# Kernel optimization log

Hardware: AMD Instinct MI355X
Metric: run time of the kernel (lower is better)

The kernel has to match this reference:

```python
import jax, jax.numpy as jnp
import numpy as np

NUM_GRAPHS = 1024  # static number of segments for global_mean_pool


def setup_inputs() -> dict:
    key = jax.random.key(0)
    ks = jax.random.split(key, 16)
    N, E, F_IN, H = 100000, 1000000, 32, 64
    NUM_ATOM, NUM_ACT, L = 16, 8, 3
    s = 0.05
    x = jax.random.normal(ks[0], (N, F_IN), dtype=jnp.float32)
    edge_index = jax.random.randint(ks[1], (2, E), 0, N, dtype=jnp.int64)
    batch = jnp.sort(jax.random.randint(ks[2], (N,), 0, NUM_GRAPHS, dtype=jnp.int64))
    W_emb = jax.random.normal(ks[3], (F_IN, H), dtype=jnp.float32) * s
    b_emb = jnp.zeros((H,), dtype=jnp.float32)
    W_convs = jax.random.normal(ks[4], (L, H, H), dtype=jnp.float32) * s
    b_convs = jnp.zeros((L, H), dtype=jnp.float32)
    W_act = jax.random.normal(ks[5], (H, NUM_ACT), dtype=jnp.float32) * s
    b_act = jnp.zeros((NUM_ACT,), dtype=jnp.float32)
    W_tgt = jax.random.normal(ks[6], (H, 1), dtype=jnp.float32) * s
    b_tgt = jnp.zeros((1,), dtype=jnp.float32)
    W_atom = jax.random.normal(ks[7], (H, NUM_ATOM), dtype=jnp.float32) * s
    b_atom = jnp.zeros((NUM_ATOM,), dtype=jnp.float32)
    return {"x": x, "edge_index": edge_index, "batch": batch,
            "W_emb": W_emb, "b_emb": b_emb, "W_convs": W_convs, "b_convs": b_convs,
            "W_act": W_act, "b_act": b_act, "W_tgt": W_tgt, "b_tgt": b_tgt,
            "W_atom": W_atom, "b_atom": b_atom}


def reference(x, edge_index, batch, W_emb, b_emb, W_convs, b_convs,
              W_act, b_act, W_tgt, b_tgt, W_atom, b_atom):
    N = x.shape[0]
    # --- GCN normalization with self-loops (PyG GCNConv default) ---
    self_idx = jnp.arange(N, dtype=edge_index.dtype)
    src = jnp.concatenate([edge_index[0], self_idx])  # message source (row)
    dst = jnp.concatenate([edge_index[1], self_idx])  # aggregation target (col)
    ones_e = jnp.ones(src.shape[0], dtype=x.dtype)
    deg = jax.ops.segment_sum(ones_e, dst, num_segments=N)  # in-degree + self-loop
    dinv = jnp.where(deg > 0, jax.lax.rsqrt(deg), 0.0)
    norm = (dinv[src] * dinv[dst])[:, None]  # [E+N, 1]

    h = jax.nn.relu(x @ W_emb + b_emb)  # node embedding
    for i in range(W_convs.shape[0]):
        m = (h @ W_convs[i])[src] * norm            # gather + scale
        agg = jax.ops.segment_sum(m, dst, num_segments=N)  # scatter-add
        h = jax.nn.relu(agg + b_convs[i])

    # --- global mean pool over graphs ---
    cnt = jax.ops.segment_sum(jnp.ones(N, dtype=x.dtype), batch, num_segments=NUM_GRAPHS)
    pooled = jax.ops.segment_sum(h, batch, num_segments=NUM_GRAPHS)
    pooled = pooled / jnp.maximum(cnt, 1.0)[:, None]

    action_type_logits = pooled @ W_act + b_act            # [G, num_action_types]
    target_node_logits = (h @ W_tgt + b_tgt)[:, 0]         # [N]
    new_atom_type_logits = pooled @ W_atom + b_atom        # [G, num_atom_types]
    return (action_type_logits, target_node_logits, new_atom_type_logits, h)
```

## Files before the change

kernel.cpp:

```cpp
#include <hip/hip_runtime.h>
#include <hip/hip_fp16.h>

#define HD 64
#define FIN 32
#define NG 1024
#define STRIDE 64
#define SLOT0 4
#define DEGCAP 59
#define SH 72

typedef _Float16 f16x8 __attribute__((ext_vector_type(8)));
typedef float f32x4 __attribute__((ext_vector_type(4)));

__device__ __forceinline__ int fmap(int jt, int c) {
    return (jt < 2) ? (2 * c + jt) : (32 + 2 * c + (jt - 2));
}

__device__ __forceinline__ void nt_store_h2(__half2 v, __half2* p) {
    __builtin_nontemporal_store(*(int*)&v, (int*)p);
}

__global__ __launch_bounds__(256) void k_prep(int* __restrict__ col,
                                              __half2* __restrict__ BaZR,
                                              __half2* __restrict__ BbZR,
                                              const float* __restrict__ Wconv,
                                              __half* __restrict__ Wf, int wtotal,
                                              const float* __restrict__ Wemb,
                                              __half* __restrict__ Wef, int N) {
    int b = blockIdx.x, t = threadIdx.x;
    int v = b * 256 + t;
    if (v < N) col[(size_t)v << 6] = 0;
    if (b < 48) {
        int tid = b * 256 + t;
        if (tid < wtotal) {
            int layer = tid >> 12;
            int r = tid & 4095;
            int frag = r >> 9, lane = (r >> 3) & 63, e = r & 7;
            int jt = frag >> 1, kh = frag & 1;
            int k = kh * 32 + (lane >> 4) * 8 + e;
            int n = fmap(jt, lane & 15);
            Wf[tid] = (_Float16)Wconv[(size_t)layer * 4096 + k * 64 + n];
        }
    } else if (b < 56) {
        int tid = (b - 48) * 256 + t;
        if (tid < 2048) {
            int jt = tid >> 9, lane = (tid >> 3) & 63, e = tid & 7;
            int k = (lane >> 4) * 8 + e;
            int n = fmap(jt, lane & 15);
            Wef[tid] = (_Float16)Wemb[k * HD + n];
        }
    } else if (b == 56) {
        __half2 z = __floats2half2_rn(0.f, 0.f);
        if (t < 32) BaZR[t] = z;
        else if (t < 64) BbZR[t - 32] = z;
    }
}

__global__ void k_fill(const int* __restrict__ src, const int* __restrict__ dst,
                       int* __restrict__ col, int E) {
    int e = blockIdx.x * blockDim.x + threadIdx.x;
    if (e < E) {
        int d = dst[e];
        int pos = atomicAdd(&col[(size_t)d << 6], 1);
        if (pos < STRIDE - SLOT0) col[((size_t)d << 6) + SLOT0 + pos] = src[e];
    }
}

__device__ __forceinline__ void gemm_from_lds(const __half* hs, const float* dvs,
                                              const float4* __restrict__ Wf4,
                                              __half2* __restrict__ Bout,
                                              int node0, int N, int t) {
    int lane = t & 63;
    int wv = t >> 6;
    int lm = lane & 15, kq = lane >> 4;
    union U { float4 f; f16x8 h; };
    U a0, a1;
    const __half* hrow = hs + (size_t)(wv * 16 + lm) * SH;
    a0.f = *(const float4*)(hrow + kq * 8);
    a1.f = *(const float4*)(hrow + 32 + kq * 8);
    f32x4 acc[4];
#pragma unroll
    for (int jt = 0; jt < 4; jt++) acc[jt] = (f32x4){0.f, 0.f, 0.f, 0.f};
#pragma unroll
    for (int jt = 0; jt < 4; jt++) {
        U b0, b1;
        b0.f = Wf4[(jt * 2 + 0) * 64 + lane];
        b1.f = Wf4[(jt * 2 + 1) * 64 + lane];
        acc[jt] = __builtin_amdgcn_mfma_f32_16x16x32_f16(a0.h, b0.h, acc[jt], 0, 0, 0);
        acc[jt] = __builtin_amdgcn_mfma_f32_16x16x32_f16(a1.h, b1.h, acc[jt], 0, 0, 0);
    }
#pragma unroll
    for (int r = 0; r < 4; r++) {
        int lv = wv * 16 + kq * 4 + r;
        int v = node0 + lv;
        if (v < N) {
            float dv = dvs[lv];
            nt_store_h2(__floats2half2_rn(acc[0][r] * dv, acc[1][r] * dv),
                        Bout + (size_t)v * 32 + lm);
            nt_store_h2(__floats2half2_rn(acc[2][r] * dv, acc[3][r] * dv),
                        Bout + (size_t)v * 32 + 16 + lm);
        }
    }
}

__global__ __launch_bounds__(256) void k_emb_gemm0(const float* __restrict__ x,
                                                   const float4* __restrict__ Wef4,
                                                   const float* __restrict__ bemb,
                                                   const int* __restrict__ col,
                                                   const float4* __restrict__ Wf0,
                                                   __half2* __restrict__ Bout, int N) {
    __shared__ __half hs[64 * SH];
    __shared__ float dvs[64];
    int t = threadIdx.x;
    int lane = t & 63;
    int wv = t >> 6;
    int node0 = blockIdx.x * 64;
    int nodew = node0 + wv * 16;
    int m = lane & 15, kq = lane >> 4;

    int vm = nodew + m;
    if (vm > N - 1) vm = N - 1;
    const float4* xr = (const float4*)(x + (size_t)vm * FIN + kq * 8);
    float4 xa = xr[0], xb = xr[1];
    f16x8 a;
    a[0] = (_Float16)xa.x; a[1] = (_Float16)xa.y; a[2] = (_Float16)xa.z; a[3] = (_Float16)xa.w;
    a[4] = (_Float16)xb.x; a[5] = (_Float16)xb.y; a[6] = (_Float16)xb.z; a[7] = (_Float16)xb.w;

    union U { float4 f; f16x8 h; };
    f32x4 acc[4];
#pragma unroll
    for (int jt = 0; jt < 4; jt++) {
        U b; b.f = Wef4[jt * 64 + lane];
        acc[jt] = (f32x4){0.f, 0.f, 0.f, 0.f};
        acc[jt] = __builtin_amdgcn_mfma_f32_16x16x32_f16(a, b.h, acc[jt], 0, 0, 0);
    }
    float b01x = bemb[2 * m], b01y = bemb[2 * m + 1];
    float b23x = bemb[32 + 2 * m], b23y = bemb[32 + 2 * m + 1];
    __half2 z = __floats2half2_rn(0.f, 0.f);
#pragma unroll
    for (int r = 0; r < 4; r++) {
        int lv = wv * 16 + kq * 4 + r;
        int v = node0 + lv;
        __half2 p01 = z, p23 = z;
        if (v < N) {
            p01 = __floats2half2_rn(fmaxf(acc[0][r] + b01x, 0.f),
                                    fmaxf(acc[1][r] + b01y, 0.f));
            p23 = __floats2half2_rn(fmaxf(acc[2][r] + b23x, 0.f),
                                    fmaxf(acc[3][r] + b23y, 0.f));
        }
        *(__half2*)(hs + (size_t)lv * SH + 2 * m) = p01;
        *(__half2*)(hs + (size_t)lv * SH + 32 + 2 * m) = p23;
        if (m == 0)
            dvs[lv] = (v < N) ? rsqrtf((float)(col[(size_t)v << 6] + 1)) : 1.f;
    }
    __syncthreads();
    gemm_from_lds(hs, dvs, Wf0, Bout, node0, N, t);
}

__global__ __launch_bounds__(256) void k_layer(const __half2* __restrict__ Bin,
                                               const int* __restrict__ col,
                                               const float* __restrict__ bias,
                                               const float4* __restrict__ Wnext,
                                               __half2* __restrict__ Bout,
                                               int N, int ZR) {
    __shared__ __half hs[64 * SH];
    __shared__ float dvs[64];
    int t = threadIdx.x;
    int lane = t & 63;
    int wv = t >> 6;
    int node0 = blockIdx.x * 64;
    int q = lane >> 4, p = lane & 15;
    float4 b4 = *(const float4*)(bias + 4 * p);

#pragma unroll
    for (int pass = 0; pass < 4; pass++) {
        int lv = wv * 16 + pass * 4 + q;
        int v = node0 + lv;
        int vc = (v < N) ? v : 0;
        const int* bucket = col + ((size_t)vc << 6);
        int degraw = bucket[0];
        int deg = degraw > DEGCAP ? DEGCAP : degraw;
        int dmax = deg;
        dmax = max(dmax, __shfl_xor(dmax, 16, 64));
        dmax = max(dmax, __shfl_xor(dmax, 32, 64));
        int rounds = (dmax + 4) >> 2;

        float2 a0 = make_float2(0.f, 0.f), a1 = make_float2(0.f, 0.f);
        for (int rd = 0; rd < rounds; rd++) {
            int4 iq = *(const int4*)(bucket + SLOT0 + rd * 4);
            int idx[4] = {iq.x, iq.y, iq.z, iq.w};
#pragma unroll
            for (int r = 0; r < 4; r++) {
                int i = rd * 4 + r;
                idx[r] = (i < deg) ? idx[r] : ((i == deg) ? vc : ZR);
            }
            float2 raw[4];
#pragma unroll
            for (int r = 0; r < 4; r++)
                raw[r] = *(const float2*)(Bin + (size_t)idx[r] * 32 + p * 2);
#pragma unroll
            for (int r = 0; r < 4; r++) {
                float2 f0 = __half22float2(((const __half2*)&raw[r])[0]);
                float2 f1 = __half22float2(((const __half2*)&raw[r])[1]);
                a0.x += f0.x; a0.y += f0.y; a1.x += f1.x; a1.y += f1.y;
            }
        }
        float dv = rsqrtf((float)(degraw + 1));
        float r0 = fmaxf(dv * a0.x + b4.x, 0.f);
        float r1 = fmaxf(dv * a0.y + b4.y, 0.f);
        float r2 = fmaxf(dv * a1.x + b4.z, 0.f);
        float r3 = fmaxf(dv * a1.y + b4.w, 0.f);
        if (v >= N) { r0 = r1 = r2 = r3 = 0.f; dv = 1.f; }
        __half* hrow = hs + (size_t)lv * SH + 4 * p;
        *(__half2*)(hrow) = __floats2half2_rn(r0, r1);
        *(__half2*)(hrow + 2) = __floats2half2_rn(r2, r3);
        if (p == 0) dvs[lv] = dv;
    }
    __syncthreads();
    gemm_from_lds(hs, dvs, Wnext, Bout, node0, N, t);
}

__global__ __launch_bounds__(256) void k_gather_last(const __half2* __restrict__ Bin,
                                                     const int* __restrict__ col,
                                                     const float* __restrict__ bias,
                                                     float* __restrict__ hout,
                                                     const float* __restrict__ Wtgt,
                                                     const float* __restrict__ btgt,
                                                     float* __restrict__ tgt,
                                                     int N, int ZR) {
    int t = threadIdx.x;
    int lane = t & 63;
    int wv = t >> 6;
    int q = lane >> 4, p = lane & 15;
    int v = blockIdx.x * 16 + wv * 4 + q;
    if (v >= N) return;

    const int* bucket = col + ((size_t)v << 6);
    int degraw = bucket[0];
    int deg = degraw > DEGCAP ? DEGCAP : degraw;
    int dmax = deg;
    dmax = max(dmax, __shfl_xor(dmax, 16, 64));
    dmax = max(dmax, __shfl_xor(dmax, 32, 64));
    int rounds = (dmax + 4) >> 2;

    float2 a0 = make_float2(0.f, 0.f), a1 = make_float2(0.f, 0.f);
    for (int rd = 0; rd < rounds; rd++) {
        int4 iq = *(const int4*)(bucket + SLOT0 + rd * 4);
        int idx[4] = {iq.x, iq.y, iq.z, iq.w};
#pragma unroll
        for (int r = 0; r < 4; r++) {
            int i = rd * 4 + r;
            idx[r] = (i < deg) ? idx[r] : ((i == deg) ? v : ZR);
        }
        float2 raw[4];
#pragma unroll
        for (int r = 0; r < 4; r++)
            raw[r] = *(const float2*)(Bin + (size_t)idx[r] * 32 + p * 2);
#pragma unroll
        for (int r = 0; r < 4; r++) {
            float2 f0 = __half22float2(((const __half2*)&raw[r])[0]);
            float2 f1 = __half22float2(((const __half2*)&raw[r])[1]);
            a0.x += f0.x; a0.y += f0.y; a1.x += f1.x; a1.y += f1.y;
        }
    }
    float dv = rsqrtf((float)(degraw + 1));
    float4 b4 = *(const float4*)(bias + 4 * p);
    float r0 = fmaxf(dv * a0.x + b4.x, 0.f);
    float r1 = fmaxf(dv * a0.y + b4.y, 0.f);
    float r2 = fmaxf(dv * a1.x + b4.z, 0.f);
    float r3 = fmaxf(dv * a1.y + b4.w, 0.f);
    f32x4 o = (f32x4){r0, r1, r2, r3};
    __builtin_nontemporal_store(o, (f32x4*)(hout + (size_t)v * HD + 4 * p));
    float4 w4 = *(const float4*)(Wtgt + 4 * p);
    float pp = r0 * w4.x + r1 * w4.y + r2 * w4.z + r3 * w4.w;
    pp += __shfl_xor(pp, 1, 64); pp += __shfl_xor(pp, 2, 64);
    pp += __shfl_xor(pp, 4, 64); pp += __shfl_xor(pp, 8, 64);
    if (p == 0) __builtin_nontemporal_store(pp + btgt[0], tgt + v);
}

__global__ __launch_bounds__(256) void k_pool(const float* __restrict__ h,
                                              const int* __restrict__ batch,
                                              const float* __restrict__ Wact,
                                              const float* __restrict__ bact,
                                              const float* __restrict__ Watom,
                                              const float* __restrict__ batom,
                                              float* __restrict__ out_act,
                                              float* __restrict__ out_atom, int N) {
    int g = blockIdx.x;
    int t = threadIdx.x;
    int q = t >> 4, p = t & 15;
    int lo = 0, hi = N;
    while (lo < hi) { int mid = (lo + hi) >> 1; if (batch[mid] < g) lo = mid + 1; else hi = mid; }
    int s = lo;
    hi = N;
    while (lo < hi) { int mid = (lo + hi) >> 1; if (batch[mid] < g + 1) lo = mid + 1; else hi = mid; }
    int e2 = lo;
    float4 acc = make_float4(0.f, 0.f, 0.f, 0.f);
    for (int v = s + q; v < e2; v += 16) {
        float4 c = *(const float4*)(h + (size_t)v * HD + p * 4);
        acc.x += c.x; acc.y += c.y; acc.z += c.z; acc.w += c.w;
    }
    __shared__ float4 part[16][16];
    part[q][p] = acc;
    __syncthreads();
    __shared__ float pl[HD];
    if (t < 16) {
        float4 tot = part[0][t];
#pragma unroll
        for (int k = 1; k < 16; k++) {
            float4 c = part[k][t];
            tot.x += c.x; tot.y += c.y; tot.z += c.z; tot.w += c.w;
        }
        float cnt = fmaxf((float)(e2 - s), 1.f);
        pl[t * 4 + 0] = tot.x / cnt; pl[t * 4 + 1] = tot.y / cnt;
        pl[t * 4 + 2] = tot.z / cnt; pl[t * 4 + 3] = tot.w / cnt;
    }
    __syncthreads();
    if (t < 8) {
        float a = bact[t];
#pragma unroll
        for (int k = 0; k < HD; k++) a += pl[k] * Wact[k * 8 + t];
        out_act[g * 8 + t] = a;
    }
    if (t < 16) {
        float a = batom[t];
#pragma unroll
        for (int k = 0; k < HD; k++) a += pl[k] * Watom[k * 16 + t];
        out_atom[g * 16 + t] = a;
    }
}

extern "C" void kernel_launch(void* const* d_in, const int* in_sizes, int n_in,
                              void* d_out, int out_size, void* d_ws, size_t ws_size,
                              hipStream_t stream) {
    const float* x     = (const float*)d_in[0];
    const int*   ei    = (const int*)d_in[1];
    const int*   batch = (const int*)d_in[2];
    const float* Wemb  = (const float*)d_in[3];
    const float* bemb  = (const float*)d_in[4];
    const float* Wconv = (const float*)d_in[5];
    const float* bconv = (const float*)d_in[6];
    const float* Wact  = (const float*)d_in[7];
    const float* bact  = (const float*)d_in[8];
    const float* Wtgt  = (const float*)d_in[9];
    const float* btgt  = (const float*)d_in[10];
    const float* Watom = (const float*)d_in[11];
    const float* batom = (const float*)d_in[12];

    const int N = in_sizes[0] / FIN;
    const int E = in_sizes[1] / 2;
    const int L = in_sizes[5] / (HD * HD);
    const int Npad = (N + 63) & ~63;
    const int ZR = Npad;

    int*     col = (int*)d_ws;
    __half2* Ba  = (__half2*)(col + ((size_t)N << 6));
    __half2* Bb  = Ba + (size_t)(Npad + 64) * 32;
    __half*  Wf  = (__half*)(Bb + (size_t)(Npad + 64) * 32);
    __half*  Wef = Wf + (size_t)L * 4096;

    const int* srcA = ei;
    const int* dstA = ei + E;

    float* out_act  = (float*)d_out;
    float* out_tgt  = out_act + (size_t)NG * 8;
    float* out_atom = out_tgt + N;
    float* out_h    = out_atom + (size_t)NG * 16;

    const int nbN = (N + 255) / 256;
    const int nbE = (E + 255) / 256;
    const int nbG = (N + 63) / 64;
    const int nbLast = (N + 15) / 16;
    const int wtotal = L * 4096;
    const int nbPrep = nbN > 57 ? nbN : 57;

    k_prep<<<nbPrep, 256, 0, stream>>>(col, Ba + (size_t)ZR * 32, Bb + (size_t)ZR * 32,
                                       Wconv, Wf, wtotal, Wemb, Wef, N);
    k_fill<<<nbE, 256, 0, stream>>>(srcA, dstA, col, E);
    k_emb_gemm0<<<nbG, 256, 0, stream>>>(x, (const float4*)Wef, bemb, col,
                                         (const float4*)Wf, Ba, N);

    __half2* cur = Ba;
    __half2* nxt = Bb;
    for (int l = 0; l < L - 1; ++l) {
        k_layer<<<nbG, 256, 0, stream>>>(cur, col, bconv + l * HD,
                                         (const float4*)(Wf + (size_t)(l + 1) * 4096),
                                         nxt, N, ZR);
        __half2* tmp = cur; cur = nxt; nxt = tmp;
    }
    k_gather_last<<<nbLast, 256, 0, stream>>>(cur, col, bconv + (size_t)(L - 1) * HD,
                                              out_h, Wtgt, btgt, out_tgt, N, ZR);
    k_pool<<<NG, 256, 0, stream>>>(out_h, batch, Wact, bact, Watom, batom,
                                   out_act, out_atom, N);
}
```

Before: 243.3 us.

## Build adjacency via binned counting sort instead of global atomic fill

Replaces the per-edge global atomic fill of the padded adjacency table with a multi-pass binning scheme. A per-block histogram of destination bins is computed, a scan produces bin offsets, edges are scattered into bins, and each bin is assembled in LDS and written out with coalesced nontemporal stores. This targets scattered global atomics and random writes, at the cost of three extra launches, a single-block scan, and an intermediate edge buffer placed in the Bb workspace.

```diff
diff --git a/kernel.cpp b/kernel.cpp
--- a/kernel.cpp
+++ b/kernel.cpp
@@ -9,8 +9,13 @@
 #define DEGCAP 59
 #define SH 72
 
+#define BINW 128
+#define NBMAX 1024
+#define EPB 8192
+
 typedef _Float16 f16x8 __attribute__((ext_vector_type(8)));
 typedef float f32x4 __attribute__((ext_vector_type(4)));
+typedef int i32x4 __attribute__((ext_vector_type(4)));
 
 __device__ __forceinline__ int fmap(int jt, int c) {
     return (jt < 2) ? (2 * c + jt) : (32 + 2 * c + (jt - 2));
@@ -20,16 +25,16 @@
     __builtin_nontemporal_store(*(int*)&v, (int*)p);
 }
 
-__global__ __launch_bounds__(256) void k_prep(int* __restrict__ col,
+__global__ __launch_bounds__(256) void k_prep(const int* __restrict__ dst,
+                                              int* __restrict__ blkHist, int E, int NBINS,
                                               __half2* __restrict__ BaZR,
                                               __half2* __restrict__ BbZR,
                                               const float* __restrict__ Wconv,
                                               __half* __restrict__ Wf, int wtotal,
                                               const float* __restrict__ Wemb,
-                                              __half* __restrict__ Wef, int N) {
+                                              __half* __restrict__ Wef) {
+    __shared__ int hist[NBMAX];
     int b = blockIdx.x, t = threadIdx.x;
-    int v = b * 256 + t;
-    if (v < N) col[(size_t)v << 6] = 0;
     if (b < 48) {
         int tid = b * 256 + t;
         if (tid < wtotal) {
@@ -54,15 +59,89 @@
         if (t < 32) BaZR[t] = z;
         else if (t < 64) BbZR[t - 32] = z;
     }
-}
-
-__global__ void k_fill(const int* __restrict__ src, const int* __restrict__ dst,
-                       int* __restrict__ col, int E) {
-    int e = blockIdx.x * blockDim.x + threadIdx.x;
-    if (e < E) {
+    int e0 = b * EPB;
+    if (e0 < E) {
+        for (int i = t; i < NBMAX; i += 256) hist[i] = 0;
+        __syncthreads();
+        int e1 = e0 + EPB; if (e1 > E) e1 = E;
+        for (int e = e0 + t; e < e1; e += 256) atomicAdd(&hist[dst[e] >> 7], 1);
+        __syncthreads();
+        for (int i = t; i < NBINS; i += 256) blkHist[b * NBMAX + i] = hist[i];
+    }
+}
+
+__global__ __launch_bounds__(1024) void k_scan(int* __restrict__ blkHist,
+                                               int* __restrict__ binStart,
+                                               int nb, int NBINS) {
+    __shared__ int s[NBMAX];
+    int t = threadIdx.x;
+    int run = 0;
+    if (t < NBINS) {
+        for (int blk = 0; blk < nb; blk++) {
+            int x = blkHist[blk * NBMAX + t];
+            blkHist[blk * NBMAX + t] = run;
+            run += x;
+        }
+    }
+    s[t] = run;
+    __syncthreads();
+    for (int off = 1; off < NBMAX; off <<= 1) {
+        int v = s[t];
+        int u = (t >= off) ? s[t - off] : 0;
+        __syncthreads();
+        s[t] = v + u;
+        __syncthreads();
+    }
+    if (t <= NBINS) binStart[t] = (t == 0) ? 0 : s[t - 1];
+}
+
+__global__ __launch_bounds__(256) void k_scatter(const int* __restrict__ src,
+                                                 const int* __restrict__ dst,
+                                                 const int* __restrict__ blkHist,
+                                                 const int* __restrict__ binStart,
+                                                 int2* __restrict__ binned,
+                                                 int E, int NBINS) {
+    __shared__ int pos[NBMAX];
+    int b = blockIdx.x, t = threadIdx.x;
+    for (int i = t; i < NBMAX; i += 256)
+        pos[i] = (i < NBINS) ? (blkHist[b * NBMAX + i] + binStart[i]) : 0;
+    __syncthreads();
+    int e0 = b * EPB;
+    int e1 = e0 + EPB; if (e1 > E) e1 = E;
+    for (int e = e0 + t; e < e1; e += 256) {
         int d = dst[e];
-        int pos = atomicAdd(&col[(size_t)d << 6], 1);
-        if (pos < STRIDE - SLOT0) col[((size_t)d << 6) + SLOT0 + pos] = src[e];
+        int p = atomicAdd(&pos[d >> 7], 1);
+        binned[p] = make_int2(src[e], d);
+    }
+}
+
+__global__ __launch_bounds__(256) void k_csr(const int2* __restrict__ binned,
+                                             const int* __restrict__ binStart,
+                                             int* __restrict__ col, int N) {
+    __shared__ int img[BINW * 64];
+    __shared__ int cnt[BINW];
+    int b = blockIdx.x, t = threadIdx.x;
+    for (int i = t; i < BINW * 64; i += 256) img[i] = 0;
+    for (int i = t; i < BINW; i += 256) cnt[i] = 0;
+    __syncthreads();
+    int s = binStart[b], e = binStart[b + 1];
+    for (int i = s + t; i < e; i += 256) {
+        int2 ed = binned[i];
+        int ld = ed.y & (BINW - 1);
+        int p = atomicAdd(&cnt[ld], 1);
+        if (p < STRIDE - SLOT0) img[ld * 64 + SLOT0 + p] = ed.x;
+    }
+    __syncthreads();
+    for (int i = t; i < BINW; i += 256) img[i * 64] = cnt[i];
+    __syncthreads();
+    int v0 = b * BINW;
+    int* out = col + ((size_t)v0 << 6);
+    for (int j = t; j < BINW * 16; j += 256) {
+        int node = v0 + (j >> 4);
+        if (node < N) {
+            i32x4 val = *(i32x4*)&img[j * 4];
+            __builtin_nontemporal_store(val, (i32x4*)(out + j * 4));
+        }
     }
 }
 
@@ -359,6 +438,10 @@
     __half*  Wf  = (__half*)(Bb + (size_t)(Npad + 64) * 32);
     __half*  Wef = Wf + (size_t)L * 4096;
 
+    int2* binned   = (int2*)Bb;
+    int*  blkHist  = (int*)((char*)Bb + (9u << 20));
+    int*  binStart = (int*)((char*)Bb + (10u << 20) + (512u << 10));
+
     const int* srcA = ei;
     const int* dstA = ei + E;
 
@@ -367,16 +450,19 @@
     float* out_atom = out_tgt + N;
     float* out_h    = out_atom + (size_t)NG * 16;
 
-    const int nbN = (N + 255) / 256;
-    const int nbE = (E + 255) / 256;
     const int nbG = (N + 63) / 64;
     const int nbLast = (N + 15) / 16;
     const int wtotal = L * 4096;
-    const int nbPrep = nbN > 57 ? nbN : 57;
-
-    k_prep<<<nbPrep, 256, 0, stream>>>(col, Ba + (size_t)ZR * 32, Bb + (size_t)ZR * 32,
-                                       Wconv, Wf, wtotal, Wemb, Wef, N);
-    k_fill<<<nbE, 256, 0, stream>>>(srcA, dstA, col, E);
+    const int nbF1 = (E + EPB - 1) / EPB;
+    const int NBINS = (N + BINW - 1) / BINW;
+    const int nbPrep = nbF1 > 57 ? nbF1 : 57;
+
+    k_prep<<<nbPrep, 256, 0, stream>>>(dstA, blkHist, E, NBINS,
+                                       Ba + (size_t)ZR * 32, Bb + (size_t)ZR * 32,
+                                       Wconv, Wf, wtotal, Wemb, Wef);
+    k_scan<<<1, 1024, 0, stream>>>(blkHist, binStart, nbF1, NBINS);
+    k_scatter<<<nbF1, 256, 0, stream>>>(srcA, dstA, blkHist, binStart, binned, E, NBINS);
+    k_csr<<<NBINS, 256, 0, stream>>>(binned, binStart, col, N);
     k_emb_gemm0<<<nbG, 256, 0, stream>>>(x, (const float4*)Wef, bemb, col,
                                          (const float4*)Wf, Ba, N);
 
```

New measurement: 265.6 us. 1.09x slower.
